# Kernel tuning notes

Hardware: AMD Instinct MI355X
Metric: run time of the kernel (lower is better)

The kernel has to match this reference:

```python
import jax, jax.numpy as jnp
import numpy as np

NEAR = 0.0
SCENE_SCALE = 1.0
OPACITY_THRESHOLD = 0.01
EARLY_TERM = 1e-4
N_RAYS = 4096
N_SAMPLES = 256
GRID = 128
FEAT = 64
HID = 128
RGB_HID = 64


def mip360_contract(c):
    # Mip-NeRF 360 scene contraction; safe norm avoids NaN grads in the unused branch.
    norm = jnp.linalg.norm(c, axis=-1, keepdims=True)
    safe = jnp.maximum(norm, 1e-12)
    return jnp.where(norm <= 1.0, c, (2.0 - 1.0 / safe) * c / safe) / 2.0


def unbounded_stepping(near, uniform_range, n):
    ts = jnp.linspace(0.0, 1.0 - 1.0 / (n + 2), n + 1)
    ts = jnp.where(ts < 0.5, 2.0 * ts, 1.0 / (2.0 - 2.0 * ts)) * uniform_range + near
    return ts[:-1], ts[1:] - ts[:-1]


def grid_sample_3d(grid, coords):
    # torch F.grid_sample bilinear, align_corners=False, zeros padding.
    # grid [D,H,W]; coords [...,3] = (x,y,z) with x->W, y->H, z->D, in [-1,1].
    D, H, W = grid.shape
    x, y, z = coords[..., 0], coords[..., 1], coords[..., 2]
    ix = ((x + 1.0) * W - 1.0) * 0.5
    iy = ((y + 1.0) * H - 1.0) * 0.5
    iz = ((z + 1.0) * D - 1.0) * 0.5
    ix0, iy0, iz0 = jnp.floor(ix), jnp.floor(iy), jnp.floor(iz)
    fx, fy, fz = ix - ix0, iy - iy0, iz - iz0
    out = jnp.zeros(x.shape, grid.dtype)
    for dz in (0, 1):
        for dy in (0, 1):
            for dx in (0, 1):
                cx, cy, cz = ix0 + dx, iy0 + dy, iz0 + dz
                w = (fx if dx else 1.0 - fx) * (fy if dy else 1.0 - fy) * (fz if dz else 1.0 - fz)
                valid = (cx >= 0) & (cx < W) & (cy >= 0) & (cy < H) & (cz >= 0) & (cz < D)
                g = grid[jnp.clip(cz, 0, D - 1).astype(jnp.int32),
                         jnp.clip(cy, 0, H - 1).astype(jnp.int32),
                         jnp.clip(cx, 0, W - 1).astype(jnp.int32)]
                out = out + jnp.where(valid, w * g, 0.0)
    return out


def setup_inputs() -> dict:
    key = jax.random.key(0)
    ks = jax.random.split(key, 8)
    rays_o = jax.random.normal(ks[0], (N_RAYS, 3), jnp.float32) * 0.3
    rd = jax.random.normal(ks[1], (N_RAYS, 3), jnp.float32)
    rays_d = rd / jnp.linalg.norm(rd, axis=-1, keepdims=True)
    grid = jax.random.uniform(ks[2], (GRID, GRID, GRID), jnp.float32)
    lin = lambda k, fan_in, shape: jax.random.normal(k, shape, jnp.float32) / np.sqrt(fan_in).astype(np.float32)
    return dict(
        rays_o=rays_o, rays_d=rays_d, grid=grid,
        f_w1=lin(ks[3], 3, (3, HID)), f_b1=jnp.zeros((HID,), jnp.float32),
        f_w2=lin(ks[4], HID, (HID, FEAT)), f_b2=jnp.zeros((FEAT,), jnp.float32),
        s_w=lin(ks[5], FEAT, (FEAT, 1)), s_b=jnp.zeros((1,), jnp.float32),
        r_w1=lin(ks[6], FEAT + 3, (FEAT + 3, RGB_HID)), r_b1=jnp.zeros((RGB_HID,), jnp.float32),
        r_w2=lin(ks[7], RGB_HID, (RGB_HID, 3)), r_b2=jnp.zeros((3,), jnp.float32),
        n_samples=N_SAMPLES,
    )


def reference(rays_o, rays_d, grid, f_w1, f_b1, f_w2, f_b2, s_w, s_b, r_w1, r_b1, r_w2, r_b2, n_samples):
    n_rays = rays_o.shape[0]
    t, dist = unbounded_stepping(NEAR, SCENE_SCALE, n_samples)               # [S], [S]
    samples = rays_o[:, None, :] + rays_d[:, None, :] * t[None, :, None]     # [R,S,3]
    samples = mip360_contract(samples)
    occ = grid_sample_3d(grid, samples)                                      # [R,S]
    mask = occ > OPACITY_THRESHOLD
    # feature module (dense compute, masked write as in samples_features[mask] = ...)
    feat = jax.nn.relu(samples @ f_w1 + f_b1) @ f_w2 + f_b2                  # [R,S,F]
    feat = jnp.where(mask[..., None], feat, 0.0)
    sigma = jnp.where(mask, jax.nn.softplus(feat @ s_w + s_b)[..., 0], 0.0)  # [R,S]
    a = -sigma * dist[None, :]
    trans = jnp.concatenate(
        [jnp.ones((n_rays, 1), a.dtype), jnp.exp(jnp.cumsum(a, axis=1))[:, :-1]], axis=1)
    weights = trans * (1.0 - jnp.exp(a))                                     # [R,S]
    mask2 = mask & (trans > EARLY_TERM)
    dirs = jnp.broadcast_to(rays_d[:, None, :], samples.shape)
    h = jax.nn.relu(jnp.concatenate([feat, dirs], axis=-1) @ r_w1 + r_b1)
    rgb = jax.nn.sigmoid(h @ r_w2 + r_b2) * weights[..., None]
    rgb = jnp.where(mask2[..., None], rgb, 0.0)
    return rgb.sum(axis=1)                                                   # [R,3]
```

## Files before the change

kernel.cpp:

```cpp
#include <hip/hip_runtime.h>
#include <hip/hip_bf16.h>
#include <math.h>
#include <stdint.h>

#define S    256
#define GN   128

typedef __attribute__((ext_vector_type(8))) short  short8;
typedef __attribute__((ext_vector_type(4))) float  floatx4;
typedef __attribute__((ext_vector_type(2))) float  float2v;

#define WS_BHI 0
#define WS_RW1 16384
#define WS_B2S 24576
#define WS_WS2 24592
#define WS_W1P 25104
#define WS_W2E 27152

__device__ __forceinline__ unsigned short bf16_rtne(float f) {
    uint32_t u = __builtin_bit_cast(uint32_t, f);
    uint32_t r = (u + 0x7fffu + ((u >> 16) & 1u)) >> 16;
    return (unsigned short)r;
}
__device__ __forceinline__ uint32_t cvt_pk_bf16(float a, float b) {
    float2 hh; hh.x = a; hh.y = b;
    __hip_bfloat162 pk = __float22bfloat162_rn(hh);
    uint32_t u; __builtin_memcpy(&u, &pk, 4);
    return u;
}

__global__ __launch_bounds__(256)
void nerf_prep(const float* __restrict__ f_w1, const float* __restrict__ f_b1,
               const float* __restrict__ f_w2, const float* __restrict__ f_b2,
               const float* __restrict__ s_w,  const float* __restrict__ s_b,
               const float* __restrict__ r_w1, const float* __restrict__ r_w2,
               unsigned char* __restrict__ ws)
{
    const int tid = threadIdx.x;
    if (tid < 128) {
        float acc = 0.0f;
        for (int n = 0; n < 64; ++n) acc += f_w2[tid * 64 + n] * s_w[n];
        ((float*)(ws + WS_WS2))[tid] = acc;
    } else if (tid == 128) {
        float acc = s_b[0];
        for (int n = 0; n < 64; ++n) acc += f_b2[n] * s_w[n];
        *(float*)(ws + WS_B2S) = acc;
    }
    {
        float* w1pk = (float*)(ws + WS_W1P);
        for (int pp = tid; pp < 64; pp += 256) {
            int k0 = 2 * pp, k1 = 2 * pp + 1;
            w1pk[pp * 8 + 0] = f_w1[k0];       w1pk[pp * 8 + 1] = f_w1[k1];
            w1pk[pp * 8 + 2] = f_w1[128 + k0]; w1pk[pp * 8 + 3] = f_w1[128 + k1];
            w1pk[pp * 8 + 4] = f_w1[256 + k0]; w1pk[pp * 8 + 5] = f_w1[256 + k1];
            w1pk[pp * 8 + 6] = f_b1[k0];       w1pk[pp * 8 + 7] = f_b1[k1];
        }
    }

    unsigned short* bhi = (unsigned short*)(ws + WS_BHI);
    for (int i = tid; i < 8192; i += 256) {
        int j = i & 7, L = (i >> 3) & 63, g = i >> 9;
        int tn = g & 3, kc = g >> 2;
        int q = L >> 4, cc = L & 15;
        int k = kc * 32 + q * 8 + j;
        bhi[i] = bf16_rtne(f_w2[k * 64 + tn * 16 + cc]);
    }
    unsigned short* rw = (unsigned short*)(ws + WS_RW1);
    for (int i = tid; i < 4096; i += 256) {
        int j = i & 7, L = (i >> 3) & 63, g = i >> 9;
        int tn = g & 3, ks = g >> 2;
        int q = L >> 4, cc = L & 15;
        int k = ks * 32 + q * 8 + j;
        rw[i] = bf16_rtne(r_w1[k * 64 + tn * 16 + cc]);
    }
    unsigned short* w2e = (unsigned short*)(ws + WS_W2E);
    for (int i = tid; i < 1024; i += 256) {
        int j = i & 7, L = (i >> 3) & 63, kf = i >> 9;
        int q = L >> 4, ch = L & 15;
        int k = kf * 32 + q * 8 + j;
        w2e[i] = (ch < 3) ? bf16_rtne(r_w2[k * 3 + ch]) : (unsigned short)0;
    }
}

__global__ __launch_bounds__(256, 4)
void nerf_mfma(const float* __restrict__ rays_o,
               const float* __restrict__ rays_d,
               const float* __restrict__ grid,
               const float* __restrict__ f_b2,
               const float* __restrict__ r_w1,
               const float* __restrict__ r_b1,
               const float* __restrict__ r_b2,
               const unsigned char* __restrict__ ws,
               float* __restrict__ out)
{
    __shared__ unsigned short fh[256 * 64];
    __shared__ float w1p[512];
    __shared__ float ws2L[128];
    __shared__ float aLds[S];
    __shared__ float maskLds[S];
    __shared__ float distLds[S];
    __shared__ float sWaveSum[4];
    __shared__ float sPart[4][3];

    const int tid   = threadIdx.x;
    const int ray   = blockIdx.x;
    const int lane  = tid & 63;
    const int wv    = tid >> 6;
    const int q     = lane >> 4;
    const int c     = lane & 15;
    const int mbase = wv * 64;
    const int d01   = 72 - ((c >> 3) << 4);

    if (tid < 128) {
        ((float4*)w1p)[tid] = ((const float4*)(ws + WS_W1P))[tid];
        ws2L[tid] = ((const float*)(ws + WS_WS2))[tid];
    }

    const float stop = 1.0f - 1.0f / (float)(S + 2);
    const float step = stop / (float)S;
    float u0 = (float)tid * step;
    float u1 = (float)(tid + 1) * step;
    float t    = (u0 < 0.5f) ? 2.0f * u0 : 1.0f / (2.0f - 2.0f * u0);
    float tn_  = (u1 < 0.5f) ? 2.0f * u1 : 1.0f / (2.0f - 2.0f * u1);
    float dist = tn_ - t;

    float ox = rays_o[ray * 3 + 0], oy = rays_o[ray * 3 + 1], oz = rays_o[ray * 3 + 2];
    float dxv = rays_d[ray * 3 + 0], dyv = rays_d[ray * 3 + 1], dzv = rays_d[ray * 3 + 2];

    float px = ox + dxv * t, py = oy + dyv * t, pz = oz + dzv * t;
    float nrm = sqrtf(px * px + py * py + pz * pz);
    float scale = (nrm <= 1.0f) ? 0.5f : (2.0f - 1.0f / nrm) / nrm * 0.5f;
    float cx = px * scale, cy = py * scale, cz = pz * scale;

    float ix = ((cx + 1.0f) * (float)GN - 1.0f) * 0.5f;
    float iy = ((cy + 1.0f) * (float)GN - 1.0f) * 0.5f;
    float iz = ((cz + 1.0f) * (float)GN - 1.0f) * 0.5f;
    float fx0 = floorf(ix), fy0 = floorf(iy), fz0 = floorf(iz);
    float fx = ix - fx0, fy = iy - fy0, fz = iz - fz0;
    int x0 = (int)fx0, y0 = (int)fy0, z0 = (int)fz0;
    int x1 = x0 + 1, y1 = y0 + 1, z1 = z0 + 1;

    float wxv[2], wyv[2], wzv[2];
    wxv[0] = (x0 >= 0) ? (1.0f - fx) : 0.0f;  wxv[1] = (x1 < GN) ? fx : 0.0f;
    wyv[0] = (y0 >= 0) ? (1.0f - fy) : 0.0f;  wyv[1] = (y1 < GN) ? fy : 0.0f;
    wzv[0] = (z0 >= 0) ? (1.0f - fz) : 0.0f;  wzv[1] = (z1 < GN) ? fz : 0.0f;
    int xc[2], yb[2], zb[2];
    xc[0] = (x0 < 0) ? 0 : x0;              xc[1] = (x1 > GN - 1) ? GN - 1 : x1;
    yb[0] = ((y0 < 0) ? 0 : y0) * GN;       yb[1] = ((y1 > GN - 1) ? GN - 1 : y1) * GN;
    zb[0] = ((z0 < 0) ? 0 : z0) * (GN*GN);  zb[1] = ((z1 > GN - 1) ? GN - 1 : z1) * (GN*GN);

    float occ = 0.0f;
    #pragma unroll
    for (int dzc = 0; dzc < 2; ++dzc)
    #pragma unroll
    for (int dyc = 0; dyc < 2; ++dyc)
    #pragma unroll
    for (int dxc = 0; dxc < 2; ++dxc) {
        float w = (wxv[dxc] * wyv[dyc]) * wzv[dzc];
        occ += w * grid[zb[dzc] + yb[dyc] + xc[dxc]];
    }
    bool maskA = occ > 0.01f;
    maskLds[tid] = maskA ? 1.0f : 0.0f;
    distLds[tid] = dist;

    __syncthreads();

    const unsigned short* __restrict__ bhiP = (const unsigned short*)(ws + WS_BHI);
    float sgv[4] = {0.0f, 0.0f, 0.0f, 0.0f};

    #pragma unroll 1
    for (int ph = 0; ph < 2; ++ph) {
        float cxs[2], cys[2], czs[2];
        #pragma unroll
        for (int tm = 0; tm < 2; ++tm) {
            int src = (ph * 2 + tm) * 16 + c;
            cxs[tm] = __shfl(cx, src, 64);
            cys[tm] = __shfl(cy, src, 64);
            czs[tm] = __shfl(cz, src, 64);
        }

        floatx4 acc[2][4];
        {
            float b2v[4];
            #pragma unroll
            for (int tn = 0; tn < 4; ++tn) b2v[tn] = f_b2[tn * 16 + c];
            #pragma unroll
            for (int tm = 0; tm < 2; ++tm)
                #pragma unroll
                for (int tn = 0; tn < 4; ++tn) {
                    floatx4 v; v[0] = b2v[tn]; v[1] = b2v[tn]; v[2] = b2v[tn]; v[3] = b2v[tn];
                    acc[tm][tn] = v;
                }
        }
        float2v sig2[2];
        sig2[0][0] = 0.0f; sig2[0][1] = 0.0f;
        sig2[1][0] = 0.0f; sig2[1][1] = 0.0f;

        #pragma unroll 2
        for (int kc = 0; kc < 4; ++kc) {
            const int k0  = kc * 32 + q * 8;
            const int pp0 = kc * 16 + q * 4;
            const float4* __restrict__ w1q4 = (const float4*)&w1p[pp0 * 8];
            float ws2r[8];
            *(float4*)(ws2r)     = *(const float4*)&ws2L[k0];
            *(float4*)(ws2r + 4) = *(const float4*)&ws2L[k0 + 4];

            uint32_t packed[2][4];
            #pragma unroll
            for (int p = 0; p < 4; ++p) {
                float4 q0 = w1q4[2 * p];
                float4 q1 = w1q4[2 * p + 1];
                float2v wx2 = {q0.x, q0.y};
                float2v wy2 = {q0.z, q0.w};
                float2v wz2 = {q1.x, q1.y};
                float2v bb2 = {q1.z, q1.w};
                float2v wsp = {ws2r[2 * p], ws2r[2 * p + 1]};
                #pragma unroll
                for (int tm = 0; tm < 2; ++tm) {
                    float2v h2 = bb2;
                    h2 = __builtin_elementwise_fma((float2v){cxs[tm], cxs[tm]}, wx2, h2);
                    h2 = __builtin_elementwise_fma((float2v){cys[tm], cys[tm]}, wy2, h2);
                    h2 = __builtin_elementwise_fma((float2v){czs[tm], czs[tm]}, wz2, h2);
                    h2 = __builtin_elementwise_max(h2, (float2v){0.0f, 0.0f});
                    sig2[tm] = __builtin_elementwise_fma(h2, wsp, sig2[tm]);
                    packed[tm][p] = cvt_pk_bf16(h2[0], h2[1]);
                }
            }
            short8 Ah[2];
            #pragma unroll
            for (int tm = 0; tm < 2; ++tm) {
                uint4 v4 = {packed[tm][0], packed[tm][1], packed[tm][2], packed[tm][3]};
                Ah[tm] = __builtin_bit_cast(short8, v4);
            }
            const int bbase = (kc * 4) * 512 + lane * 8;
            #pragma unroll
            for (int tn = 0; tn < 4; ++tn) {
                short8 bh = *(const short8*)(bhiP + bbase + tn * 512);
                #pragma unroll
                for (int tm = 0; tm < 2; ++tm)
                    acc[tm][tn] = __builtin_amdgcn_mfma_f32_16x16x32_bf16(Ah[tm], bh, acc[tm][tn], 0, 0, 0);
            }
        }

        #pragma unroll
        for (int tm = 0; tm < 2; ++tm)
            #pragma unroll
            for (int tn = 0; tn < 4; ++tn)
                #pragma unroll
                for (int pr = 0; pr < 2; ++pr) {
                    uint32_t u = cvt_pk_bf16(acc[tm][tn][2 * pr], acc[tm][tn][2 * pr + 1]);
                    int m0 = mbase + (ph * 2 + tm) * 16 + q * 4 + 2 * pr;
                    int i0 = m0 * 64 + c + (((tn * 2) ^ (m0 & 7)) << 3);
                    fh[i0]       = (unsigned short)u;
                    fh[i0 + d01] = (unsigned short)(u >> 16);
                }
        {
            float s0 = sig2[0][0] + sig2[0][1];
            s0 += __shfl_xor(s0, 16);
            s0 += __shfl_xor(s0, 32);
            float s1 = sig2[1][0] + sig2[1][1];
            s1 += __shfl_xor(s1, 16);
            s1 += __shfl_xor(s1, 32);
            if (ph == 0) { sgv[0] = s0; sgv[1] = s1; }
            else         { sgv[2] = s0; sgv[3] = s1; }
        }
    }

    {
        float b2s = *(const float*)(ws + WS_B2S);
        if (q == 0) {
            #pragma unroll
            for (int tm = 0; tm < 4; ++tm) {
                int m = mbase + tm * 16 + c;
                float sa = sgv[tm] + b2s;
                float sg = (maskLds[m] > 0.5f)
                         ? (fmaxf(sa, 0.0f) + __logf(1.0f + __expf(-fabsf(sa)))) : 0.0f;
                aLds[m] = -sg * distLds[m];
            }
        }
    }
    __builtin_amdgcn_wave_barrier();

    float hd[4];
    #pragma unroll
    for (int tn = 0; tn < 4; ++tn) {
        int n = tn * 16 + c;
        hd[tn] = r_b1[n] + dxv * r_w1[64 * 64 + n] + dyv * r_w1[65 * 64 + n] + dzv * r_w1[66 * 64 + n];
    }

    float av = aLds[tid];
    float v = av;
    #pragma unroll
    for (int off = 1; off < 64; off <<= 1) {
        float u2 = __shfl_up(v, off);
        if (lane >= off) v += u2;
    }
    if (lane == 63) sWaveSum[wv] = v;
    __syncthreads();
    float basev = 0.0f;
    #pragma unroll
    for (int w = 0; w < 4; ++w) basev += (w < wv) ? sWaveSum[w] : 0.0f;
    float excl = __shfl_up(v, 1);
    if (lane == 0) excl = 0.0f;
    float cum    = basev + excl;
    float trans  = __expf(cum);
    float weight = trans * (1.0f - __expf(av));
    bool  mask2  = (maskLds[tid] > 0.5f) && (trans > 1e-4f);

    const unsigned short* __restrict__ rwP = (const unsigned short*)(ws + WS_RW1);

    #pragma unroll 1
    for (int ph = 0; ph < 2; ++ph) {
        short8 afr[2][2];
        #pragma unroll
        for (int tm = 0; tm < 2; ++tm)
            #pragma unroll
            for (int ks = 0; ks < 2; ++ks) {
                int m = mbase + (ph * 2 + tm) * 16 + c;
                int gl = ks * 4 + q;
                afr[tm][ks] = *(const short8*)&fh[m * 64 + ((gl ^ (m & 7)) << 3)];
            }

        floatx4 acc[2][4];
        #pragma unroll
        for (int tm = 0; tm < 2; ++tm)
            #pragma unroll
            for (int tn = 0; tn < 4; ++tn) {
                floatx4 z; z[0] = 0.0f; z[1] = 0.0f; z[2] = 0.0f; z[3] = 0.0f;
                acc[tm][tn] = z;
            }
        #pragma unroll
        for (int ks = 0; ks < 2; ++ks)
            #pragma unroll
            for (int tn = 0; tn < 4; ++tn) {
                short8 rb = *(const short8*)(rwP + ((ks * 4 + tn) * 64 + lane) * 8);
                #pragma unroll
                for (int tm = 0; tm < 2; ++tm)
                    acc[tm][tn] = __builtin_amdgcn_mfma_f32_16x16x32_bf16(afr[tm][ks], rb, acc[tm][tn], 0, 0, 0);
            }

        __builtin_amdgcn_wave_barrier();
        #pragma unroll
        for (int tm = 0; tm < 2; ++tm)
            #pragma unroll
            for (int tn = 0; tn < 4; ++tn)
                #pragma unroll
                for (int pr = 0; pr < 2; ++pr) {
                    float2v a2 = {acc[tm][tn][2 * pr], acc[tm][tn][2 * pr + 1]};
                    a2 = a2 + (float2v){hd[tn], hd[tn]};
                    a2 = __builtin_elementwise_max(a2, (float2v){0.0f, 0.0f});
                    uint32_t u = cvt_pk_bf16(a2[0], a2[1]);
                    int m0 = mbase + (ph * 2 + tm) * 16 + q * 4 + 2 * pr;
                    int i0 = m0 * 64 + c + (((tn * 2) ^ (m0 & 7)) << 3);
                    fh[i0]       = (unsigned short)u;
                    fh[i0 + d01] = (unsigned short)(u >> 16);
                }
    }
    __builtin_amdgcn_wave_barrier();

    aLds[tid] = mask2 ? weight : 0.0f;
    __builtin_amdgcn_wave_barrier();

    const unsigned short* __restrict__ w2eP = (const unsigned short*)(ws + WS_W2E);
    short8 w2f[2];
    w2f[0] = *(const short8*)(w2eP + (0 * 64 + lane) * 8);
    w2f[1] = *(const short8*)(w2eP + (1 * 64 + lane) * 8);

    floatx4 eacc[4];
    #pragma unroll
    for (int tn = 0; tn < 4; ++tn) {
        floatx4 z; z[0] = 0.0f; z[1] = 0.0f; z[2] = 0.0f; z[3] = 0.0f;
        eacc[tn] = z;
    }
    #pragma unroll
    for (int kf = 0; kf < 2; ++kf)
        #pragma unroll
        for (int tn = 0; tn < 4; ++tn) {
            int m = mbase + tn * 16 + c;
            int gl = kf * 4 + q;
            short8 hb = *(const short8*)&fh[m * 64 + ((gl ^ (m & 7)) << 3)];
            eacc[tn] = __builtin_amdgcn_mfma_f32_16x16x32_bf16(w2f[kf], hb, eacc[tn], 0, 0, 0);
        }

    float r = 0.0f, g = 0.0f, b = 0.0f;
    if (q == 0) {
        float rb0 = r_b2[0], rb1 = r_b2[1], rb2v = r_b2[2];
        #pragma unroll
        for (int tn = 0; tn < 4; ++tn) {
            int m = mbase + tn * 16 + c;
            float wgt = aLds[m];
            r += wgt / (1.0f + __expf(-(eacc[tn][0] + rb0)));
            g += wgt / (1.0f + __expf(-(eacc[tn][1] + rb1)));
            b += wgt / (1.0f + __expf(-(eacc[tn][2] + rb2v)));
        }
    }
    #pragma unroll
    for (int off = 8; off > 0; off >>= 1) {
        r += __shfl_xor(r, off);
        g += __shfl_xor(g, off);
        b += __shfl_xor(b, off);
    }
    if (lane == 0) { sPart[wv][0] = r; sPart[wv][1] = g; sPart[wv][2] = b; }
    __syncthreads();
    if (tid == 0) {
        out[ray * 3 + 0] = sPart[0][0] + sPart[1][0] + sPart[2][0] + sPart[3][0];
        out[ray * 3 + 1] = sPart[0][1] + sPart[1][1] + sPart[2][1] + sPart[3][1];
        out[ray * 3 + 2] = sPart[0][2] + sPart[1][2] + sPart[2][2] + sPart[3][2];
    }
}

extern "C" void kernel_launch(void* const* d_in, const int* in_sizes, int n_in,
                              void* d_out, int out_size, void* d_ws, size_t ws_size,
                              hipStream_t stream) {
    const int n_rays = in_sizes[0] / 3;
    nerf_prep<<<1, 256, 0, stream>>>(
        (const float*)d_in[3], (const float*)d_in[4], (const float*)d_in[5],
        (const float*)d_in[6], (const float*)d_in[7], (const float*)d_in[8],
        (const float*)d_in[9], (const float*)d_in[11], (unsigned char*)d_ws);
    nerf_mfma<<<n_rays, 256, 0, stream>>>(
        (const float*)d_in[0],  (const float*)d_in[1],  (const float*)d_in[2],
        (const float*)d_in[6],  (const float*)d_in[9],  (const float*)d_in[10],
        (const float*)d_in[12],
        (const unsigned char*)d_ws, (float*)d_out);
}
```

Before: 171.0 us.

## Shrink LDS footprint to fit five blocks per CU

Removes the separate shared arrays for weights, mask, dist, and partial sums by aliasing the small weight tables into the feature buffer, keeping per-sample values in registers, and exchanging weights with shuffles. The wave prefix sums are passed through the output buffer in global memory instead of LDS. With LDS down to the 32KB feature buffer, the launch bound asks for 5 blocks per CU instead of 4 to hide latency better. The costs are an extra block-wide barrier before the aliased region is overwritten, a global-memory round trip for the scan partials, and tighter register limits that may cause spills.

```diff
diff --git a/kernel.cpp b/kernel.cpp
--- a/kernel.cpp
+++ b/kernel.cpp
@@ -82,7 +82,7 @@
     }
 }
 
-__global__ __launch_bounds__(256, 4)
+__global__ __launch_bounds__(256, 5)
 void nerf_mfma(const float* __restrict__ rays_o,
                const float* __restrict__ rays_d,
                const float* __restrict__ grid,
@@ -93,14 +93,8 @@
                const unsigned char* __restrict__ ws,
                float* __restrict__ out)
 {
-    __shared__ unsigned short fh[256 * 64];
-    __shared__ float w1p[512];
-    __shared__ float ws2L[128];
-    __shared__ float aLds[S];
-    __shared__ float maskLds[S];
-    __shared__ float distLds[S];
-    __shared__ float sWaveSum[4];
-    __shared__ float sPart[4][3];
+    __shared__ __align__(16) unsigned short fh[256 * 64];
+    unsigned char* fhB = (unsigned char*)fh;
 
     const int tid   = threadIdx.x;
     const int ray   = blockIdx.x;
@@ -112,8 +106,8 @@
     const int d01   = 72 - ((c >> 3) << 4);
 
     if (tid < 128) {
-        ((float4*)w1p)[tid] = ((const float4*)(ws + WS_W1P))[tid];
-        ws2L[tid] = ((const float*)(ws + WS_WS2))[tid];
+        ((float4*)(fhB + 4096))[tid] = ((const float4*)(ws + WS_W1P))[tid];
+        ((float*)(fhB + 6144))[tid]  = ((const float*)(ws + WS_WS2))[tid];
     }
 
     const float stop = 1.0f - 1.0f / (float)(S + 2);
@@ -160,8 +154,6 @@
         occ += w * grid[zb[dzc] + yb[dyc] + xc[dxc]];
     }
     bool maskA = occ > 0.01f;
-    maskLds[tid] = maskA ? 1.0f : 0.0f;
-    distLds[tid] = dist;
 
     __syncthreads();
 
@@ -200,10 +192,10 @@
         for (int kc = 0; kc < 4; ++kc) {
             const int k0  = kc * 32 + q * 8;
             const int pp0 = kc * 16 + q * 4;
-            const float4* __restrict__ w1q4 = (const float4*)&w1p[pp0 * 8];
+            const float4* w1q4 = (const float4*)(fhB + 4096 + pp0 * 32);
             float ws2r[8];
-            *(float4*)(ws2r)     = *(const float4*)&ws2L[k0];
-            *(float4*)(ws2r + 4) = *(const float4*)&ws2L[k0 + 4];
+            *(float4*)(ws2r)     = *(const float4*)(fhB + 6144 + k0 * 4);
+            *(float4*)(ws2r + 4) = *(const float4*)(fhB + 6144 + k0 * 4 + 16);
 
             uint32_t packed[2][4];
             #pragma unroll
@@ -241,6 +233,8 @@
                     acc[tm][tn] = __builtin_amdgcn_mfma_f32_16x16x32_bf16(Ah[tm], bh, acc[tm][tn], 0, 0, 0);
             }
         }
+
+        if (ph == 1) __syncthreads();
 
         #pragma unroll
         for (int tm = 0; tm < 2; ++tm)
@@ -266,20 +260,15 @@
         }
     }
 
+    float av;
     {
         float b2s = *(const float*)(ws + WS_B2S);
-        if (q == 0) {
-            #pragma unroll
-            for (int tm = 0; tm < 4; ++tm) {
-                int m = mbase + tm * 16 + c;
-                float sa = sgv[tm] + b2s;
-                float sg = (maskLds[m] > 0.5f)
-                         ? (fmaxf(sa, 0.0f) + __logf(1.0f + __expf(-fabsf(sa)))) : 0.0f;
-                aLds[m] = -sg * distLds[m];
-            }
-        }
-    }
-    __builtin_amdgcn_wave_barrier();
+        float s01  = (q & 1) ? sgv[1] : sgv[0];
+        float s23  = (q & 1) ? sgv[3] : sgv[2];
+        float sa = ((q & 2) ? s23 : s01) + b2s;
+        float sg = maskA ? (fmaxf(sa, 0.0f) + __logf(1.0f + __expf(-fabsf(sa)))) : 0.0f;
+        av = -sg * dist;
+    }
 
     float hd[4];
     #pragma unroll
@@ -288,24 +277,25 @@
         hd[tn] = r_b1[n] + dxv * r_w1[64 * 64 + n] + dyv * r_w1[65 * 64 + n] + dzv * r_w1[66 * 64 + n];
     }
 
-    float av = aLds[tid];
     float v = av;
     #pragma unroll
     for (int off = 1; off < 64; off <<= 1) {
         float u2 = __shfl_up(v, off);
         if (lane >= off) v += u2;
     }
-    if (lane == 63) sWaveSum[wv] = v;
+    if (lane == 63 && wv < 3) out[ray * 3 + wv] = v;
     __syncthreads();
-    float basev = 0.0f;
-    #pragma unroll
-    for (int w = 0; w < 4; ++w) basev += (w < wv) ? sWaveSum[w] : 0.0f;
+    float sw0 = out[ray * 3 + 0];
+    float sw1 = out[ray * 3 + 1];
+    float sw2 = out[ray * 3 + 2];
+    float basev = ((wv > 0) ? sw0 : 0.0f) + ((wv > 1) ? sw1 : 0.0f)
+                + ((wv > 2) ? sw2 : 0.0f);
     float excl = __shfl_up(v, 1);
     if (lane == 0) excl = 0.0f;
     float cum    = basev + excl;
     float trans  = __expf(cum);
     float weight = trans * (1.0f - __expf(av));
-    bool  mask2  = (maskLds[tid] > 0.5f) && (trans > 1e-4f);
+    bool  mask2  = maskA && (trans > 1e-4f);
 
     const unsigned short* __restrict__ rwP = (const unsigned short*)(ws + WS_RW1);
 
@@ -358,8 +348,10 @@
     }
     __builtin_amdgcn_wave_barrier();
 
-    aLds[tid] = mask2 ? weight : 0.0f;
-    __builtin_amdgcn_wave_barrier();
+    float wm = mask2 ? weight : 0.0f;
+    float wgt[4];
+    #pragma unroll
+    for (int tn = 0; tn < 4; ++tn) wgt[tn] = __shfl(wm, tn * 16 + c, 64);
 
     const unsigned short* __restrict__ w2eP = (const unsigned short*)(ws + WS_W2E);
     short8 w2f[2];
@@ -387,11 +379,10 @@
         float rb0 = r_b2[0], rb1 = r_b2[1], rb2v = r_b2[2];
         #pragma unroll
         for (int tn = 0; tn < 4; ++tn) {
-            int m = mbase + tn * 16 + c;
-            float wgt = aLds[m];
-            r += wgt / (1.0f + __expf(-(eacc[tn][0] + rb0)));
-            g += wgt / (1.0f + __expf(-(eacc[tn][1] + rb1)));
-            b += wgt / (1.0f + __expf(-(eacc[tn][2] + rb2v)));
+            float wgtv = wgt[tn];
+            r += wgtv / (1.0f + __expf(-(eacc[tn][0] + rb0)));
+            g += wgtv / (1.0f + __expf(-(eacc[tn][1] + rb1)));
+            b += wgtv / (1.0f + __expf(-(eacc[tn][2] + rb2v)));
         }
     }
     #pragma unroll
@@ -400,12 +391,16 @@
         g += __shfl_xor(g, off);
         b += __shfl_xor(b, off);
     }
-    if (lane == 0) { sPart[wv][0] = r; sPart[wv][1] = g; sPart[wv][2] = b; }
+    if (lane == 0) {
+        float* pp = (float*)fhB + wv * 2048;
+        pp[0] = r; pp[1] = g; pp[2] = b;
+    }
     __syncthreads();
     if (tid == 0) {
-        out[ray * 3 + 0] = sPart[0][0] + sPart[1][0] + sPart[2][0] + sPart[3][0];
-        out[ray * 3 + 1] = sPart[0][1] + sPart[1][1] + sPart[2][1] + sPart[3][1];
-        out[ray * 3 + 2] = sPart[0][2] + sPart[1][2] + sPart[2][2] + sPart[3][2];
+        float* pf = (float*)fhB;
+        out[ray * 3 + 0] = pf[0] + pf[2048] + pf[4096] + pf[6144];
+        out[ray * 3 + 1] = pf[1] + pf[2049] + pf[4097] + pf[6145];
+        out[ray * 3 + 2] = pf[2] + pf[2050] + pf[4098] + pf[6146];
     }
 }
 
```

After: 213.4 us. 24.8% more time.
